# Kernel optimization log

Hardware: AMD Instinct MI355X
Metric: run time of the kernel (lower is better)

Reference implementation:

```python
import jax, jax.numpy as jnp
import numpy as np

M = 16384          # test points
N = 16384          # train points
D = 2              # (kx, ky)
CHUNK = 8192       # rows of K_star per chunk (matches torch default)


def setup_inputs() -> dict:
    key = jax.random.key(0)
    k1, k2, k3 = jax.random.split(key, 3)
    X_test = jax.random.normal(k1, (M, D), dtype=jnp.float32)
    X_train = jax.random.normal(k2, (N, D), dtype=jnp.float32)
    alpha = jax.random.normal(k3, (N, 2), dtype=jnp.float32)  # dual vars [Re, Im]
    log_lengthscale = jnp.asarray(np.log(0.1), dtype=jnp.float32)
    log_outputscale = jnp.asarray(np.log(1.0), dtype=jnp.float32)
    return {
        "X_test": X_test,
        "X_train": X_train,
        "alpha": alpha,
        "log_lengthscale": log_lengthscale,
        "log_outputscale": log_outputscale,
    }


def reference(X_test, X_train, alpha, log_lengthscale, log_outputscale):
    """Posterior mean mu* = K_rbf(X_test, X_train) @ alpha, chunked over test rows."""
    ell2 = jnp.exp(log_lengthscale) ** 2
    sf2 = jnp.exp(log_outputscale) ** 2
    xt_sq = jnp.sum(X_train * X_train, axis=1)  # (N,)

    def chunk_fn(xc):  # xc: (CHUNK, D)
        # squared euclidean distances (clamped at 0 for numerical safety)
        sq = (jnp.sum(xc * xc, axis=1)[:, None]
              + xt_sq[None, :]
              - 2.0 * (xc @ X_train.T))          # (CHUNK, N)
        sq = jnp.maximum(sq, 0.0)
        K = sf2 * jnp.exp(-0.5 * sq / ell2)      # RBF kernel values
        return K @ alpha                          # (CHUNK, 2)

    m = X_test.shape[0]
    chunks = X_test.reshape(m // CHUNK, CHUNK, D)
    out = jax.lax.map(chunk_fn, chunks)           # (m//CHUNK, CHUNK, 2)
    return out.reshape(m, 2)
```

## Files before the change

### kernel.cpp

```cpp
#include <hip/hip_runtime.h>
#include <math.h>

#define M_PTS 16384
#define N_PTS 16384

#define NC 42
#define NCELLS (NC * NC)
#define NPAIR (NCELLS / 2)
#define H 0.25f
#define INV_H 4.0f
#define ORIG (-5.25f)
#define TCUT 20.0f
#define KMAX 7
#define MAXROWS 16
#define NWAVES (M_PTS / 64)
#define CHUNK 1024
#define MAX_ITEMS 4096

#define OFF_NITEMS 0
#define OFF_TRCUR 64
#define OFF_TECUR (OFF_TRCUR + NCELLS * 4)
#define OFF_SROW  (OFF_TECUR + NCELLS * 4)
#define OFF_SPRE  (OFF_SROW + NWAVES * MAXROWS * 4)
#define OFF_ITEMS (OFF_SPRE + NWAVES * (MAXROWS + 1) * 4)
#define OFF_TRA   ((OFF_ITEMS + MAX_ITEMS * 4 + 255) & ~255)
#define OFF_TRW1  (OFF_TRA + N_PTS * 16)
#define OFF_T4    (OFF_TRW1 + N_PTS * 4)
#define WS_NEED   (OFF_T4 + (size_t)M_PTS * 16)

__device__ __forceinline__ float fexp2(float x) {
#if __has_builtin(__builtin_amdgcn_exp2f)
    return __builtin_amdgcn_exp2f(x);
#else
    return exp2f(x);
#endif
}

__device__ __forceinline__ void gatomic_fadd(float* p, float v) {
    asm volatile("global_atomic_add_f32 %0, %1, off" :: "v"(p), "v"(v) : "memory");
}

__device__ __forceinline__ int cellco(float v) {
    int c = (int)floorf((v - ORIG) * INV_H);
    return min(NC - 1, max(0, c));
}

__global__ __launch_bounds__(1024) void prep_kernel(
        const float2* __restrict__ Xtr, const float2* __restrict__ Xte,
        const float* __restrict__ log_ell,
        int* __restrict__ trcur, int* __restrict__ tecur,
        int* __restrict__ sRowG, int* __restrict__ sPreG,
        int* __restrict__ items, int* __restrict__ nitemsG) {
    __shared__ int hTr[NCELLS], hTe[NCELLS];
    __shared__ int sc[1024];
    __shared__ int trsL[NCELLS + 1], PL[NCELLS + 1];
    const int tid = threadIdx.x;

    if (tid == 0) nitemsG[0] = 0;
    for (int i = tid; i < NCELLS; i += 1024) { hTr[i] = 0; hTe[i] = 0; }
    __syncthreads();
    for (int i = tid; i < N_PTS; i += 1024) {
        float2 t = Xtr[i];
        atomicAdd(&hTr[cellco(t.y) * NC + cellco(t.x)], 1);
        float2 x = Xte[i];
        atomicAdd(&hTe[cellco(x.y) * NC + cellco(x.x)], 1);
    }
    __syncthreads();

    int pv = (tid < NPAIR) ? (hTr[2 * tid] + hTr[2 * tid + 1]) : 0;
    sc[tid] = pv; __syncthreads();
    for (int off = 1; off < 1024; off <<= 1) {
        int u = (tid >= off) ? sc[tid - off] : 0;
        __syncthreads(); sc[tid] += u; __syncthreads();
    }
    if (tid < NPAIR) {
        int e = sc[tid] - pv;
        trsL[2 * tid] = e;
        trsL[2 * tid + 1] = e + hTr[2 * tid];
    }
    if (tid == NPAIR - 1) trsL[NCELLS] = sc[tid];
    __syncthreads();

    pv = (tid < NPAIR) ? (hTe[2 * tid] + hTe[2 * tid + 1]) : 0;
    sc[tid] = pv; __syncthreads();
    for (int off = 1; off < 1024; off <<= 1) {
        int u = (tid >= off) ? sc[tid - off] : 0;
        __syncthreads(); sc[tid] += u; __syncthreads();
    }
    if (tid < NPAIR) {
        int e = sc[tid] - pv;
        PL[2 * tid] = e;
        PL[2 * tid + 1] = e + hTe[2 * tid];
    }
    if (tid == NPAIR - 1) PL[NCELLS] = sc[tid];
    __syncthreads();

    for (int c = tid; c < NCELLS; c += 1024) {
        trcur[c] = trsL[c];
        tecur[c] = PL[c];
    }

    if (tid < NWAVES) {
        const int w = tid;
        const float ell = expf(log_ell[0]);
        const float cmag = 0.5f / (ell * ell) * 1.4426950408889634f;
        const float r2 = TCUT / cmag;
        const int K = (int)floorf(sqrtf(r2) * INV_H) + 1;

        int clo, chi;
        {
            int s = w * 64, lo = 0, hi = NCELLS;
            while (lo + 1 < hi) { int m = (lo + hi) >> 1; if (PL[m] <= s) lo = m; else hi = m; }
            clo = lo;
            s = w * 64 + 63; lo = 0; hi = NCELLS;
            while (lo + 1 < hi) { int m = (lo + hi) >> 1; if (PL[m] <= s) lo = m; else hi = m; }
            chi = lo;
        }
        const int rl = clo / NC, cl = clo % NC;
        const int rh = chi / NC, ch = chi % NC;
        int wlo = max(0, rl - K), whi = min(NC - 1, rh + K);
        int nr = whi - wlo + 1;
        bool full = (K > KMAX) || (nr > MAXROWS);

        int pre = 0;
        if (full) {
            sRowG[w * MAXROWS] = 0;
            sPreG[w * (MAXROWS + 1)] = 0;
            pre = N_PTS;
            for (int i = 1; i <= MAXROWS; ++i) sPreG[w * (MAXROWS + 1) + i] = N_PTS;
        } else {
            const bool single = (rl == rh);
            const int cmin = single ? cl : 0;
            const int cmax = single ? ch : (NC - 1);
            sPreG[w * (MAXROWS + 1)] = 0;
            int idx = 0;
            for (int wr = wlo; wr <= whi; ++wr, ++idx) {
                int dy = (wr < rl) ? (rl - wr) : ((wr > rh) ? (wr - rh) : 0);
                int kx;
                if (dy <= 1) kx = K;
                else {
                    float d = (float)(dy - 1) * H;
                    kx = (int)floorf(sqrtf(fmaxf(r2 - d * d, 0.f)) * INV_H) + 1;
                }
                int c0 = max(0, cmin - kx);
                int c1 = min(NC - 1, cmax + kx);
                int js = trsL[wr * NC + c0];
                int je = trsL[wr * NC + c1 + 1];
                sRowG[w * MAXROWS + idx] = js - pre;
                pre += je - js;
                sPreG[w * (MAXROWS + 1) + idx + 1] = pre;
            }
            for (; idx < MAXROWS; ++idx)
                sPreG[w * (MAXROWS + 1) + idx + 1] = pre;
        }
        const int nch = (pre + CHUNK - 1) / CHUNK;
        for (int k = 0; k < nch; ++k) {
            int slot = atomicAdd(nitemsG, 1);
            items[slot] = w | (k << 16);
        }
    }
}

__global__ void scatter_kernel(const float2* __restrict__ Xtr,
                               const float2* __restrict__ Xte,
                               const float2* __restrict__ alpha,
                               const float* __restrict__ log_ell,
                               const float* __restrict__ log_sf,
                               int* __restrict__ trcur, int* __restrict__ tecur,
                               float4* __restrict__ trA, float* __restrict__ trW1,
                               float4* __restrict__ T4, float2* __restrict__ out2) {
    int i = blockIdx.x * blockDim.x + threadIdx.x;
    if (i >= N_PTS) return;
    out2[i] = make_float2(0.f, 0.f);
    float ell = expf(log_ell[0]);
    float sf2 = expf(2.0f * log_sf[0]);
    float c = -0.5f / (ell * ell) * 1.4426950408889634f;

    float2 t = Xtr[i];
    float2 a = alpha[i];
    int ct = cellco(t.y) * NC + cellco(t.x);
    int pt = atomicAdd(&trcur[ct], 1);
    trA[pt] = make_float4(-2.f * c * t.x, -2.f * c * t.y,
                          c * (t.x * t.x + t.y * t.y), sf2 * a.x);
    trW1[pt] = sf2 * a.y;

    float2 x = Xte[i];
    int cx = cellco(x.y) * NC + cellco(x.x);
    int px = atomicAdd(&tecur[cx], 1);
    T4[px] = make_float4(x.x, x.y, c * (x.x * x.x + x.y * x.y),
                         __int_as_float(i));
}

__global__ __launch_bounds__(256) void gp_main(
        const float4* __restrict__ T4, const float4* __restrict__ trA,
        const float* __restrict__ trW1, const int* __restrict__ sRowG,
        const int* __restrict__ sPreG, const int* __restrict__ items,
        const int* __restrict__ nitemsG, float* __restrict__ out) {
    const int nit = nitemsG[0];
    if ((int)blockIdx.x >= nit) return;
    const int item = items[blockIdx.x];
    const int w = item & 0xFFFF;
    const int k = item >> 16;

    __shared__ float4 sA[CHUNK];
    __shared__ __align__(16) float sW[CHUNK];
    __shared__ float2 red[4][64];
    __shared__ int off[MAXROWS];
    __shared__ int pre[MAXROWS + 1];

    const int tid = threadIdx.x;
    const int p = tid >> 6;
    const int lane = tid & 63;

    if (tid < MAXROWS) off[tid] = sRowG[w * MAXROWS + tid];
    if (tid < MAXROWS + 1) pre[tid] = sPreG[w * (MAXROWS + 1) + tid];

    float4 tp = T4[w * 64 + lane];
    const float x = tp.x, y = tp.y, b = tp.z;
    const int oi = __float_as_int(tp.w);
    __syncthreads();

    const int total = pre[MAXROWS];
    const int base0 = k << 10;
    const int n = min(CHUNK, total - base0);

    {
        int r = 0;
        for (int g = tid; g < CHUNK; g += 256) {
            float4 tv; float wv;
            if (g < n) {
                int gg = base0 + g;
                while (gg >= pre[r + 1]) ++r;
                int j = gg + off[r];
                tv = trA[j];
                wv = trW1[j];
            } else {
                tv = make_float4(0.f, 0.f, -1.0e30f, 0.f);
                wv = 0.f;
            }
            sA[g] = tv;
            sW[g] = wv;
        }
    }
    __syncthreads();

    float a0 = 0.f, a1 = 0.f;
#pragma unroll 2
    for (int q = p; q < CHUNK / 4; q += 4) {
        float4 t0 = sA[4 * q];
        float4 t1 = sA[4 * q + 1];
        float4 t2 = sA[4 * q + 2];
        float4 t3 = sA[4 * q + 3];
        float4 wv = *(const float4*)&sW[4 * q];
        float e0 = fexp2(fmaf(t0.x, x, fmaf(t0.y, y, b + t0.z)));
        float e1 = fexp2(fmaf(t1.x, x, fmaf(t1.y, y, b + t1.z)));
        float e2 = fexp2(fmaf(t2.x, x, fmaf(t2.y, y, b + t2.z)));
        float e3 = fexp2(fmaf(t3.x, x, fmaf(t3.y, y, b + t3.z)));
        a0 = fmaf(e0, t0.w, a0); a1 = fmaf(e0, wv.x, a1);
        a0 = fmaf(e1, t1.w, a0); a1 = fmaf(e1, wv.y, a1);
        a0 = fmaf(e2, t2.w, a0); a1 = fmaf(e2, wv.z, a1);
        a0 = fmaf(e3, t3.w, a0); a1 = fmaf(e3, wv.w, a1);
    }

    red[p][lane] = make_float2(a0, a1);
    __syncthreads();
    if (p == 0) {
        float s0 = 0.f, s1 = 0.f;
#pragma unroll
        for (int q = 0; q < 4; ++q) {
            float2 v = red[q][lane];
            s0 += v.x; s1 += v.y;
        }
        if (s0 != 0.f || s1 != 0.f) {
            gatomic_fadd(&out[2 * oi], s0);
            gatomic_fadd(&out[2 * oi + 1], s1);
        }
    }
}

__global__ __launch_bounds__(256, 8) void gp_dense(
        const float2* __restrict__ Xte, const float2* __restrict__ Xtr,
        const float2* __restrict__ alpha, const float* __restrict__ log_ell,
        const float* __restrict__ log_sf, float* __restrict__ out) {
    __shared__ float4 sSt[128];
    __shared__ float sA1[128];
    const int tid = threadIdx.x;
    const float ell = expf(log_ell[0]);
    const float c = -0.5f / (ell * ell) * 1.4426950408889634f;
    const int j0 = blockIdx.y * 128;
    if (tid < 128) {
        const float sf2 = expf(2.0f * log_sf[0]);
        float2 t = Xtr[j0 + tid];
        float2 a = alpha[j0 + tid];
        sSt[tid] = make_float4(-2.f * c * t.x, -2.f * c * t.y,
                               c * (t.x * t.x + t.y * t.y), sf2 * a.x);
        sA1[tid] = sf2 * a.y;
    }
    const int base = blockIdx.x * 1024 + tid;
    float2 x0 = Xte[base], x1 = Xte[base + 256];
    float2 x2 = Xte[base + 512], x3 = Xte[base + 768];
    const float b0 = c * (x0.x * x0.x + x0.y * x0.y);
    const float b1 = c * (x1.x * x1.x + x1.y * x1.y);
    const float b2 = c * (x2.x * x2.x + x2.y * x2.y);
    const float b3 = c * (x3.x * x3.x + x3.y * x3.y);
    __syncthreads();
    float a00 = 0.f, a01 = 0.f, a10 = 0.f, a11 = 0.f;
    float a20 = 0.f, a21 = 0.f, a30 = 0.f, a31 = 0.f;
#pragma unroll 2
    for (int j = 0; j < 128; ++j) {
        float4 s = sSt[j];
        float w1 = sA1[j];
        float e0 = fexp2(fminf(fmaf(s.x, x0.x, fmaf(s.y, x0.y, b0 + s.z)), 0.f));
        float e1 = fexp2(fminf(fmaf(s.x, x1.x, fmaf(s.y, x1.y, b1 + s.z)), 0.f));
        float e2 = fexp2(fminf(fmaf(s.x, x2.x, fmaf(s.y, x2.y, b2 + s.z)), 0.f));
        float e3 = fexp2(fminf(fmaf(s.x, x3.x, fmaf(s.y, x3.y, b3 + s.z)), 0.f));
        a00 = fmaf(e0, s.w, a00); a01 = fmaf(e0, w1, a01);
        a10 = fmaf(e1, s.w, a10); a11 = fmaf(e1, w1, a11);
        a20 = fmaf(e2, s.w, a20); a21 = fmaf(e2, w1, a21);
        a30 = fmaf(e3, s.w, a30); a31 = fmaf(e3, w1, a31);
    }
    gatomic_fadd(&out[2 * base], a00);            gatomic_fadd(&out[2 * base + 1], a01);
    gatomic_fadd(&out[2 * (base + 256)], a10);    gatomic_fadd(&out[2 * (base + 256) + 1], a11);
    gatomic_fadd(&out[2 * (base + 512)], a20);    gatomic_fadd(&out[2 * (base + 512) + 1], a21);
    gatomic_fadd(&out[2 * (base + 768)], a30);    gatomic_fadd(&out[2 * (base + 768) + 1], a31);
}

extern "C" void kernel_launch(void* const* d_in, const int* in_sizes, int n_in,
                              void* d_out, int out_size, void* d_ws, size_t ws_size,
                              hipStream_t stream) {
    const float2* Xte = (const float2*)d_in[0];
    const float2* Xtr = (const float2*)d_in[1];
    const float2* alpha = (const float2*)d_in[2];
    const float* log_ell = (const float*)d_in[3];
    const float* log_sf = (const float*)d_in[4];
    float* out = (float*)d_out;

    if (ws_size >= WS_NEED) {
        char* ws = (char*)d_ws;
        int* nitems = (int*)(ws + OFF_NITEMS);
        int* trcur = (int*)(ws + OFF_TRCUR);
        int* tecur = (int*)(ws + OFF_TECUR);
        int* sRowG = (int*)(ws + OFF_SROW);
        int* sPreG = (int*)(ws + OFF_SPRE);
        int* items = (int*)(ws + OFF_ITEMS);
        float4* trA = (float4*)(ws + OFF_TRA);
        float* trW1 = (float*)(ws + OFF_TRW1);
        float4* T4 = (float4*)(ws + OFF_T4);

        prep_kernel<<<1, 1024, 0, stream>>>(Xtr, Xte, log_ell, trcur, tecur,
                                            sRowG, sPreG, items, nitems);
        scatter_kernel<<<N_PTS / 256, 256, 0, stream>>>(
            Xtr, Xte, alpha, log_ell, log_sf, trcur, tecur, trA, trW1, T4,
            (float2*)out);
        gp_main<<<MAX_ITEMS, 256, 0, stream>>>(T4, trA, trW1, sRowG, sPreG,
                                               items, nitems, out);
    } else {
        hipMemsetAsync(out, 0, (size_t)out_size * sizeof(float), stream);
        dim3 grid(M_PTS / 1024, N_PTS / 128);
        gp_dense<<<grid, 256, 0, stream>>>(Xte, Xtr, alpha, log_ell, log_sf, out);
    }
}
```

Measured before the change: 115.7 us.

## Fuse prep, scatter and main into one persistent kernel with grid barriers

Replaces the three-kernel pipeline (single-block prep, scatter, per-item main) with one persistent kernel of 256 blocks of 1024 threads, using atomic-counter grid barriers between the histogram, prefix/plan, scatter and compute phases. The histograms move to global memory and are zeroed by a memset. Work items are now grid-strided over the persistent blocks, and each block uses 16 waves per chunk instead of 4. This removes launch gaps and the serial single-block prep launch, but relies on all 256 blocks being co-resident, and the compute phase now does a full-block reduction for every item.

```diff
diff --git a/kernel.cpp b/kernel.cpp
--- a/kernel.cpp
+++ b/kernel.cpp
@@ -3,6 +3,8 @@
 
 #define M_PTS 16384
 #define N_PTS 16384
+#define NB 256
+#define NT 1024
 
 #define NC 42
 #define NCELLS (NC * NC)
@@ -13,20 +15,24 @@
 #define TCUT 20.0f
 #define KMAX 7
 #define MAXROWS 16
-#define NWAVES (M_PTS / 64)
+#define NTW (M_PTS / 64)
 #define CHUNK 1024
 #define MAX_ITEMS 4096
 
-#define OFF_NITEMS 0
-#define OFF_TRCUR 64
+#define OFF_BAR 0
+#define OFF_NITEMS 32
+#define OFF_HTR 64
+#define OFF_HTE (OFF_HTR + NCELLS * 4)
+#define ZERO_BYTES (OFF_HTE + NCELLS * 4)
+#define OFF_TRCUR ZERO_BYTES
 #define OFF_TECUR (OFF_TRCUR + NCELLS * 4)
-#define OFF_SROW  (OFF_TECUR + NCELLS * 4)
-#define OFF_SPRE  (OFF_SROW + NWAVES * MAXROWS * 4)
-#define OFF_ITEMS (OFF_SPRE + NWAVES * (MAXROWS + 1) * 4)
-#define OFF_TRA   ((OFF_ITEMS + MAX_ITEMS * 4 + 255) & ~255)
-#define OFF_TRW1  (OFF_TRA + N_PTS * 16)
-#define OFF_T4    (OFF_TRW1 + N_PTS * 4)
-#define WS_NEED   (OFF_T4 + (size_t)M_PTS * 16)
+#define OFF_SROW (OFF_TECUR + NCELLS * 4)
+#define OFF_SPRE (OFF_SROW + NTW * MAXROWS * 4)
+#define OFF_ITEMS (OFF_SPRE + NTW * (MAXROWS + 1) * 4)
+#define OFF_TRA ((OFF_ITEMS + MAX_ITEMS * 4 + 255) & ~255)
+#define OFF_TRW1 (OFF_TRA + N_PTS * 16)
+#define OFF_T4 (OFF_TRW1 + N_PTS * 4)
+#define WS_NEED (OFF_T4 + (size_t)M_PTS * 16)
 
 __device__ __forceinline__ float fexp2(float x) {
 #if __has_builtin(__builtin_amdgcn_exp2f)
@@ -45,191 +51,185 @@
     return min(NC - 1, max(0, c));
 }
 
-__global__ __launch_bounds__(1024) void prep_kernel(
-        const float2* __restrict__ Xtr, const float2* __restrict__ Xte,
-        const float* __restrict__ log_ell,
-        int* __restrict__ trcur, int* __restrict__ tecur,
-        int* __restrict__ sRowG, int* __restrict__ sPreG,
-        int* __restrict__ items, int* __restrict__ nitemsG) {
-    __shared__ int hTr[NCELLS], hTe[NCELLS];
+__device__ __forceinline__ void gbar(int* bar, int idx) {
+    __syncthreads();
+    if (threadIdx.x == 0) {
+        __threadfence();
+        atomicAdd(&bar[idx], 1);
+        while (__hip_atomic_load(&bar[idx], __ATOMIC_RELAXED,
+                                 __HIP_MEMORY_SCOPE_AGENT) < NB)
+            __builtin_amdgcn_s_sleep(2);
+        __threadfence();
+    }
+    __syncthreads();
+}
+
+__global__ __launch_bounds__(NT) void gp_fused(
+        const float2* __restrict__ Xte, const float2* __restrict__ Xtr,
+        const float2* __restrict__ alpha, const float* __restrict__ log_ell,
+        const float* __restrict__ log_sf,
+        int* bar, int* nitemsG, int* hTr, int* hTe,
+        int* trcur, int* tecur, int* sRowG, int* sPreG, int* items,
+        float4* trA, float* trW1, float4* T4, float* out) {
     __shared__ int sc[1024];
-    __shared__ int trsL[NCELLS + 1], PL[NCELLS + 1];
+    __shared__ int trsL[NCELLS + 1];
+    __shared__ int PL[NCELLS + 1];
+    __shared__ float4 sA[CHUNK];
+    __shared__ __align__(16) float sW[CHUNK];
+    __shared__ float2 red[16][64];
+    __shared__ int off[MAXROWS];
+    __shared__ int pre[MAXROWS + 1];
+
     const int tid = threadIdx.x;
-
-    if (tid == 0) nitemsG[0] = 0;
-    for (int i = tid; i < NCELLS; i += 1024) { hTr[i] = 0; hTe[i] = 0; }
-    __syncthreads();
-    for (int i = tid; i < N_PTS; i += 1024) {
+    const int bid = blockIdx.x;
+
+    if (tid < 64) {
+        int i = bid * 64 + tid;
         float2 t = Xtr[i];
         atomicAdd(&hTr[cellco(t.y) * NC + cellco(t.x)], 1);
         float2 x = Xte[i];
         atomicAdd(&hTe[cellco(x.y) * NC + cellco(x.x)], 1);
     }
-    __syncthreads();
-
-    int pv = (tid < NPAIR) ? (hTr[2 * tid] + hTr[2 * tid + 1]) : 0;
-    sc[tid] = pv; __syncthreads();
-    for (int off = 1; off < 1024; off <<= 1) {
-        int u = (tid >= off) ? sc[tid - off] : 0;
-        __syncthreads(); sc[tid] += u; __syncthreads();
-    }
-    if (tid < NPAIR) {
-        int e = sc[tid] - pv;
-        trsL[2 * tid] = e;
-        trsL[2 * tid + 1] = e + hTr[2 * tid];
-    }
-    if (tid == NPAIR - 1) trsL[NCELLS] = sc[tid];
-    __syncthreads();
-
-    pv = (tid < NPAIR) ? (hTe[2 * tid] + hTe[2 * tid + 1]) : 0;
-    sc[tid] = pv; __syncthreads();
-    for (int off = 1; off < 1024; off <<= 1) {
-        int u = (tid >= off) ? sc[tid - off] : 0;
-        __syncthreads(); sc[tid] += u; __syncthreads();
-    }
-    if (tid < NPAIR) {
-        int e = sc[tid] - pv;
-        PL[2 * tid] = e;
-        PL[2 * tid + 1] = e + hTe[2 * tid];
-    }
-    if (tid == NPAIR - 1) PL[NCELLS] = sc[tid];
-    __syncthreads();
-
-    for (int c = tid; c < NCELLS; c += 1024) {
-        trcur[c] = trsL[c];
-        tecur[c] = PL[c];
-    }
-
-    if (tid < NWAVES) {
-        const int w = tid;
-        const float ell = expf(log_ell[0]);
-        const float cmag = 0.5f / (ell * ell) * 1.4426950408889634f;
-        const float r2 = TCUT / cmag;
-        const int K = (int)floorf(sqrtf(r2) * INV_H) + 1;
-
-        int clo, chi;
-        {
-            int s = w * 64, lo = 0, hi = NCELLS;
-            while (lo + 1 < hi) { int m = (lo + hi) >> 1; if (PL[m] <= s) lo = m; else hi = m; }
-            clo = lo;
-            s = w * 64 + 63; lo = 0; hi = NCELLS;
-            while (lo + 1 < hi) { int m = (lo + hi) >> 1; if (PL[m] <= s) lo = m; else hi = m; }
-            chi = lo;
-        }
-        const int rl = clo / NC, cl = clo % NC;
-        const int rh = chi / NC, ch = chi % NC;
-        int wlo = max(0, rl - K), whi = min(NC - 1, rh + K);
-        int nr = whi - wlo + 1;
-        bool full = (K > KMAX) || (nr > MAXROWS);
-
-        int pre = 0;
-        if (full) {
-            sRowG[w * MAXROWS] = 0;
-            sPreG[w * (MAXROWS + 1)] = 0;
-            pre = N_PTS;
-            for (int i = 1; i <= MAXROWS; ++i) sPreG[w * (MAXROWS + 1) + i] = N_PTS;
-        } else {
-            const bool single = (rl == rh);
-            const int cmin = single ? cl : 0;
-            const int cmax = single ? ch : (NC - 1);
-            sPreG[w * (MAXROWS + 1)] = 0;
-            int idx = 0;
-            for (int wr = wlo; wr <= whi; ++wr, ++idx) {
-                int dy = (wr < rl) ? (rl - wr) : ((wr > rh) ? (wr - rh) : 0);
-                int kx;
-                if (dy <= 1) kx = K;
-                else {
-                    float d = (float)(dy - 1) * H;
-                    kx = (int)floorf(sqrtf(fmaxf(r2 - d * d, 0.f)) * INV_H) + 1;
+    gbar(bar, 0);
+
+    if (bid == 0) {
+        int v = (tid < NPAIR) ? (hTr[2 * tid] + hTr[2 * tid + 1]) : 0;
+        sc[tid] = v; __syncthreads();
+        for (int o = 1; o < 1024; o <<= 1) {
+            int u = (tid >= o) ? sc[tid - o] : 0;
+            __syncthreads(); sc[tid] += u; __syncthreads();
+        }
+        if (tid < NPAIR) {
+            int e = sc[tid] - v;
+            trsL[2 * tid] = e;
+            trsL[2 * tid + 1] = e + hTr[2 * tid];
+        }
+        if (tid == NPAIR - 1) trsL[NCELLS] = sc[tid];
+        __syncthreads();
+        v = (tid < NPAIR) ? (hTe[2 * tid] + hTe[2 * tid + 1]) : 0;
+        sc[tid] = v; __syncthreads();
+        for (int o = 1; o < 1024; o <<= 1) {
+            int u = (tid >= o) ? sc[tid - o] : 0;
+            __syncthreads(); sc[tid] += u; __syncthreads();
+        }
+        if (tid < NPAIR) {
+            int e = sc[tid] - v;
+            PL[2 * tid] = e;
+            PL[2 * tid + 1] = e + hTe[2 * tid];
+        }
+        if (tid == NPAIR - 1) PL[NCELLS] = sc[tid];
+        __syncthreads();
+
+        for (int c = tid; c < NCELLS; c += NT) {
+            trcur[c] = trsL[c];
+            tecur[c] = PL[c];
+        }
+
+        if (tid < NTW) {
+            const int w = tid;
+            const float ell = expf(log_ell[0]);
+            const float cmag = 0.5f / (ell * ell) * 1.4426950408889634f;
+            const float r2 = TCUT / cmag;
+            const int K = (int)floorf(sqrtf(r2) * INV_H) + 1;
+
+            int clo, chi;
+            {
+                int s = w * 64, lo = 0, hi = NCELLS;
+                while (lo + 1 < hi) { int m = (lo + hi) >> 1; if (PL[m] <= s) lo = m; else hi = m; }
+                clo = lo;
+                s = w * 64 + 63; lo = 0; hi = NCELLS;
+                while (lo + 1 < hi) { int m = (lo + hi) >> 1; if (PL[m] <= s) lo = m; else hi = m; }
+                chi = lo;
+            }
+            const int rl = clo / NC, cl = clo % NC;
+            const int rh = chi / NC, ch = chi % NC;
+            int wlo = max(0, rl - K), whi = min(NC - 1, rh + K);
+            int nr = whi - wlo + 1;
+            bool full = (K > KMAX) || (nr > MAXROWS);
+
+            int preAcc = 0;
+            if (full) {
+                sRowG[w * MAXROWS] = 0;
+                sPreG[w * (MAXROWS + 1)] = 0;
+                preAcc = N_PTS;
+                for (int i = 1; i <= MAXROWS; ++i)
+                    sPreG[w * (MAXROWS + 1) + i] = N_PTS;
+            } else {
+                const bool single = (rl == rh);
+                const int cmin = single ? cl : 0;
+                const int cmax = single ? ch : (NC - 1);
+                sPreG[w * (MAXROWS + 1)] = 0;
+                int idx = 0;
+                for (int wr = wlo; wr <= whi; ++wr, ++idx) {
+                    int dy = (wr < rl) ? (rl - wr) : ((wr > rh) ? (wr - rh) : 0);
+                    int kx;
+                    if (dy <= 1) kx = K;
+                    else {
+                        float d = (float)(dy - 1) * H;
+                        kx = (int)floorf(sqrtf(fmaxf(r2 - d * d, 0.f)) * INV_H) + 1;
+                    }
+                    int c0 = max(0, cmin - kx);
+                    int c1 = min(NC - 1, cmax + kx);
+                    int js = trsL[wr * NC + c0];
+                    int je = trsL[wr * NC + c1 + 1];
+                    sRowG[w * MAXROWS + idx] = js - preAcc;
+                    preAcc += je - js;
+                    sPreG[w * (MAXROWS + 1) + idx + 1] = preAcc;
                 }
-                int c0 = max(0, cmin - kx);
-                int c1 = min(NC - 1, cmax + kx);
-                int js = trsL[wr * NC + c0];
-                int je = trsL[wr * NC + c1 + 1];
-                sRowG[w * MAXROWS + idx] = js - pre;
-                pre += je - js;
-                sPreG[w * (MAXROWS + 1) + idx + 1] = pre;
-            }
-            for (; idx < MAXROWS; ++idx)
-                sPreG[w * (MAXROWS + 1) + idx + 1] = pre;
-        }
-        const int nch = (pre + CHUNK - 1) / CHUNK;
-        for (int k = 0; k < nch; ++k) {
-            int slot = atomicAdd(nitemsG, 1);
-            items[slot] = w | (k << 16);
-        }
-    }
-}
-
-__global__ void scatter_kernel(const float2* __restrict__ Xtr,
-                               const float2* __restrict__ Xte,
-                               const float2* __restrict__ alpha,
-                               const float* __restrict__ log_ell,
-                               const float* __restrict__ log_sf,
-                               int* __restrict__ trcur, int* __restrict__ tecur,
-                               float4* __restrict__ trA, float* __restrict__ trW1,
-                               float4* __restrict__ T4, float2* __restrict__ out2) {
-    int i = blockIdx.x * blockDim.x + threadIdx.x;
-    if (i >= N_PTS) return;
-    out2[i] = make_float2(0.f, 0.f);
-    float ell = expf(log_ell[0]);
-    float sf2 = expf(2.0f * log_sf[0]);
-    float c = -0.5f / (ell * ell) * 1.4426950408889634f;
-
-    float2 t = Xtr[i];
-    float2 a = alpha[i];
-    int ct = cellco(t.y) * NC + cellco(t.x);
-    int pt = atomicAdd(&trcur[ct], 1);
-    trA[pt] = make_float4(-2.f * c * t.x, -2.f * c * t.y,
-                          c * (t.x * t.x + t.y * t.y), sf2 * a.x);
-    trW1[pt] = sf2 * a.y;
-
-    float2 x = Xte[i];
-    int cx = cellco(x.y) * NC + cellco(x.x);
-    int px = atomicAdd(&tecur[cx], 1);
-    T4[px] = make_float4(x.x, x.y, c * (x.x * x.x + x.y * x.y),
-                         __int_as_float(i));
-}
-
-__global__ __launch_bounds__(256) void gp_main(
-        const float4* __restrict__ T4, const float4* __restrict__ trA,
-        const float* __restrict__ trW1, const int* __restrict__ sRowG,
-        const int* __restrict__ sPreG, const int* __restrict__ items,
-        const int* __restrict__ nitemsG, float* __restrict__ out) {
+                for (; idx < MAXROWS; ++idx)
+                    sPreG[w * (MAXROWS + 1) + idx + 1] = preAcc;
+            }
+            const int nch = (preAcc + CHUNK - 1) / CHUNK;
+            int slot = atomicAdd(nitemsG, nch);
+            for (int k = 0; k < nch; ++k)
+                items[slot + k] = w | (k << 16);
+        }
+    }
+    gbar(bar, 1);
+
+    if (tid < 64) {
+        int i = bid * 64 + tid;
+        ((float2*)out)[i] = make_float2(0.f, 0.f);
+        float ell = expf(log_ell[0]);
+        float sf2 = expf(2.0f * log_sf[0]);
+        float c = -0.5f / (ell * ell) * 1.4426950408889634f;
+
+        float2 t = Xtr[i];
+        float2 a = alpha[i];
+        int ct = cellco(t.y) * NC + cellco(t.x);
+        int pt = atomicAdd(&trcur[ct], 1);
+        trA[pt] = make_float4(-2.f * c * t.x, -2.f * c * t.y,
+                              c * (t.x * t.x + t.y * t.y), sf2 * a.x);
+        trW1[pt] = sf2 * a.y;
+
+        float2 x = Xte[i];
+        int cx = cellco(x.y) * NC + cellco(x.x);
+        int px = atomicAdd(&tecur[cx], 1);
+        T4[px] = make_float4(x.x, x.y, c * (x.x * x.x + x.y * x.y),
+                             __int_as_float(i));
+    }
+    gbar(bar, 2);
+
     const int nit = nitemsG[0];
-    if ((int)blockIdx.x >= nit) return;
-    const int item = items[blockIdx.x];
-    const int w = item & 0xFFFF;
-    const int k = item >> 16;
-
-    __shared__ float4 sA[CHUNK];
-    __shared__ __align__(16) float sW[CHUNK];
-    __shared__ float2 red[4][64];
-    __shared__ int off[MAXROWS];
-    __shared__ int pre[MAXROWS + 1];
-
-    const int tid = threadIdx.x;
     const int p = tid >> 6;
     const int lane = tid & 63;
-
-    if (tid < MAXROWS) off[tid] = sRowG[w * MAXROWS + tid];
-    if (tid < MAXROWS + 1) pre[tid] = sPreG[w * (MAXROWS + 1) + tid];
-
-    float4 tp = T4[w * 64 + lane];
-    const float x = tp.x, y = tp.y, b = tp.z;
-    const int oi = __float_as_int(tp.w);
-    __syncthreads();
-
-    const int total = pre[MAXROWS];
-    const int base0 = k << 10;
-    const int n = min(CHUNK, total - base0);
-
-    {
-        int r = 0;
-        for (int g = tid; g < CHUNK; g += 256) {
+    for (int it = bid; it < nit; it += NB) {
+        const int item = items[it];
+        const int w = item & 0xFFFF;
+        const int k = item >> 16;
+        if (tid < MAXROWS) off[tid] = sRowG[w * MAXROWS + tid];
+        if (tid < MAXROWS + 1) pre[tid] = sPreG[w * (MAXROWS + 1) + tid];
+        float4 tp = T4[w * 64 + lane];
+        __syncthreads();
+
+        const int total = pre[MAXROWS];
+        const int base0 = k << 10;
+        const int n = min(CHUNK, total - base0);
+        {
             float4 tv; float wv;
-            if (g < n) {
-                int gg = base0 + g;
+            if (tid < n) {
+                int gg = base0 + tid;
+                int r = 0;
                 while (gg >= pre[r + 1]) ++r;
                 int j = gg + off[r];
                 tv = trA[j];
@@ -238,43 +238,45 @@
                 tv = make_float4(0.f, 0.f, -1.0e30f, 0.f);
                 wv = 0.f;
             }
-            sA[g] = tv;
-            sW[g] = wv;
-        }
-    }
-    __syncthreads();
-
-    float a0 = 0.f, a1 = 0.f;
+            sA[tid] = tv;
+            sW[tid] = wv;
+        }
+        __syncthreads();
+
+        const float x = tp.x, y = tp.y, b = tp.z;
+        const int oi = __float_as_int(tp.w);
+        float a0 = 0.f, a1 = 0.f;
 #pragma unroll 2
-    for (int q = p; q < CHUNK / 4; q += 4) {
-        float4 t0 = sA[4 * q];
-        float4 t1 = sA[4 * q + 1];
-        float4 t2 = sA[4 * q + 2];
-        float4 t3 = sA[4 * q + 3];
-        float4 wv = *(const float4*)&sW[4 * q];
-        float e0 = fexp2(fmaf(t0.x, x, fmaf(t0.y, y, b + t0.z)));
-        float e1 = fexp2(fmaf(t1.x, x, fmaf(t1.y, y, b + t1.z)));
-        float e2 = fexp2(fmaf(t2.x, x, fmaf(t2.y, y, b + t2.z)));
-        float e3 = fexp2(fmaf(t3.x, x, fmaf(t3.y, y, b + t3.z)));
-        a0 = fmaf(e0, t0.w, a0); a1 = fmaf(e0, wv.x, a1);
-        a0 = fmaf(e1, t1.w, a0); a1 = fmaf(e1, wv.y, a1);
-        a0 = fmaf(e2, t2.w, a0); a1 = fmaf(e2, wv.z, a1);
-        a0 = fmaf(e3, t3.w, a0); a1 = fmaf(e3, wv.w, a1);
-    }
-
-    red[p][lane] = make_float2(a0, a1);
-    __syncthreads();
-    if (p == 0) {
-        float s0 = 0.f, s1 = 0.f;
+        for (int q = p; q < CHUNK / 4; q += 16) {
+            float4 t0 = sA[4 * q];
+            float4 t1 = sA[4 * q + 1];
+            float4 t2 = sA[4 * q + 2];
+            float4 t3 = sA[4 * q + 3];
+            float4 wv = *(const float4*)&sW[4 * q];
+            float e0 = fexp2(fmaf(t0.x, x, fmaf(t0.y, y, b + t0.z)));
+            float e1 = fexp2(fmaf(t1.x, x, fmaf(t1.y, y, b + t1.z)));
+            float e2 = fexp2(fmaf(t2.x, x, fmaf(t2.y, y, b + t2.z)));
+            float e3 = fexp2(fmaf(t3.x, x, fmaf(t3.y, y, b + t3.z)));
+            a0 = fmaf(e0, t0.w, a0); a1 = fmaf(e0, wv.x, a1);
+            a0 = fmaf(e1, t1.w, a0); a1 = fmaf(e1, wv.y, a1);
+            a0 = fmaf(e2, t2.w, a0); a1 = fmaf(e2, wv.z, a1);
+            a0 = fmaf(e3, t3.w, a0); a1 = fmaf(e3, wv.w, a1);
+        }
+        red[p][lane] = make_float2(a0, a1);
+        __syncthreads();
+        if (p == 0) {
+            float s0 = 0.f, s1 = 0.f;
 #pragma unroll
-        for (int q = 0; q < 4; ++q) {
-            float2 v = red[q][lane];
-            s0 += v.x; s1 += v.y;
-        }
-        if (s0 != 0.f || s1 != 0.f) {
-            gatomic_fadd(&out[2 * oi], s0);
-            gatomic_fadd(&out[2 * oi + 1], s1);
-        }
+            for (int q = 0; q < 16; ++q) {
+                float2 vq = red[q][lane];
+                s0 += vq.x; s1 += vq.y;
+            }
+            if (s0 != 0.f || s1 != 0.f) {
+                gatomic_fadd(&out[2 * oi], s0);
+                gatomic_fadd(&out[2 * oi + 1], s1);
+            }
+        }
+        __syncthreads();
     }
 }
 
@@ -337,7 +339,10 @@
 
     if (ws_size >= WS_NEED) {
         char* ws = (char*)d_ws;
+        int* bar = (int*)(ws + OFF_BAR);
         int* nitems = (int*)(ws + OFF_NITEMS);
+        int* hTr = (int*)(ws + OFF_HTR);
+        int* hTe = (int*)(ws + OFF_HTE);
         int* trcur = (int*)(ws + OFF_TRCUR);
         int* tecur = (int*)(ws + OFF_TECUR);
         int* sRowG = (int*)(ws + OFF_SROW);
@@ -347,13 +352,10 @@
         float* trW1 = (float*)(ws + OFF_TRW1);
         float4* T4 = (float4*)(ws + OFF_T4);
 
-        prep_kernel<<<1, 1024, 0, stream>>>(Xtr, Xte, log_ell, trcur, tecur,
-                                            sRowG, sPreG, items, nitems);
-        scatter_kernel<<<N_PTS / 256, 256, 0, stream>>>(
-            Xtr, Xte, alpha, log_ell, log_sf, trcur, tecur, trA, trW1, T4,
-            (float2*)out);
-        gp_main<<<MAX_ITEMS, 256, 0, stream>>>(T4, trA, trW1, sRowG, sPreG,
-                                               items, nitems, out);
+        hipMemsetAsync(ws, 0, ZERO_BYTES, stream);
+        gp_fused<<<NB, NT, 0, stream>>>(Xte, Xtr, alpha, log_ell, log_sf,
+                                        bar, nitems, hTr, hTe, trcur, tecur,
+                                        sRowG, sPreG, items, trA, trW1, T4, out);
     } else {
         hipMemsetAsync(out, 0, (size_t)out_size * sizeof(float), stream);
         dim3 grid(M_PTS / 1024, N_PTS / 128);
```

New measurement: 155.7 us. +34.7%, slower.
